# Performance work log

Hardware: AMD Instinct MI355X
Metric: run time of the kernel (lower is better)

## Reference

```python
import jax, jax.numpy as jnp
import numpy as np

N_NODES = 50000
N_EDGES = 800000
IN_FEATS = 256
OUT_FEATS = 64


def setup_inputs() -> dict:
    key = jax.random.key(0)
    k1, k2, k3, k4, k5 = jax.random.split(key, 5)
    h = jax.random.normal(k1, (N_NODES, IN_FEATS), dtype=jnp.float32)
    norm = jax.random.uniform(k2, (N_NODES,), dtype=jnp.float32)
    src = jax.random.randint(k3, (N_EDGES,), 0, N_NODES, dtype=jnp.int32)
    dst = jax.random.randint(k4, (N_EDGES,), 0, N_NODES, dtype=jnp.int32)
    # xavier_uniform for weight [in, out]
    limit = float(np.sqrt(6.0 / (IN_FEATS + OUT_FEATS)))
    weight = jax.random.uniform(k5, (IN_FEATS, OUT_FEATS), dtype=jnp.float32,
                                minval=-limit, maxval=limit)
    bias = jnp.zeros((OUT_FEATS,), dtype=jnp.float32)
    return {"h": h, "norm": norm, "src": src, "dst": dst,
            "weight": weight, "bias": bias}


def reference(h, norm, src, dst, weight, bias):
    # h: [N, in], weight: [in, out] -> projected node features [N, out]
    hw = jnp.matmul(h, weight)
    # message per edge: h_src * norm_src  -> [E, out]
    msg = hw[src] * norm[src][:, None]
    # sum over in-neighbors of each dst node -> [N, out]
    agg = jax.ops.segment_sum(msg, dst, num_segments=N_NODES)
    # scale by dst norm, add bias, activation
    out = agg * norm[:, None] + bias
    return jax.nn.relu(out)
```

## Files before the change

### kernel.cpp

```cpp
#include <hip/hip_runtime.h>

#define K_FEATS 256
#define C_FEATS 64
#define RCHUNK 1024
#define RROUNDS (RCHUNK / 64)
#define NDIGIT 512
#define DSHIFT 7
#define NMASK 127
#define LCAP 2560

typedef __attribute__((ext_vector_type(8))) short short8;
typedef __attribute__((ext_vector_type(8))) unsigned short ushort8;
typedef __attribute__((ext_vector_type(4))) float f32x4;

__device__ __forceinline__ unsigned short f2bf(float f) {
    union { float f; unsigned u; } v; v.f = f;
    unsigned r = v.u + 0x7FFF + ((v.u >> 16) & 1);
    return (unsigned short)(r >> 16);
}

__device__ __forceinline__ float bflo(unsigned u) { return __uint_as_float(u << 16); }
__device__ __forceinline__ float bfhi(unsigned u) { return __uint_as_float(u & 0xFFFF0000u); }


__global__ __launch_bounds__(256) void packhist_w_kernel(
    const int* __restrict__ dst, unsigned short* __restrict__ cm16,
    const float* __restrict__ w, unsigned short* __restrict__ wt,
    int n_edges, int nchunk)
{
    const int tid = threadIdx.x;
    if ((int)blockIdx.x < nchunk) {
        __shared__ unsigned cnt[NDIGIT];
        #pragma unroll
        for (int j = 0; j < NDIGIT / 256; ++j) cnt[tid + j * 256] = 0;
        __syncthreads();
        const int e0 = blockIdx.x * RCHUNK + tid * 4;
        if (e0 + 3 < n_edges) {
            const int4 d4 = *reinterpret_cast<const int4*>(dst + e0);
            atomicAdd(&cnt[d4.x >> DSHIFT], 1);
            atomicAdd(&cnt[d4.y >> DSHIFT], 1);
            atomicAdd(&cnt[d4.z >> DSHIFT], 1);
            atomicAdd(&cnt[d4.w >> DSHIFT], 1);
        } else {
            #pragma unroll
            for (int j = 0; j < 4; ++j) {
                if (e0 + j < n_edges) atomicAdd(&cnt[dst[e0 + j] >> DSHIFT], 1);
            }
        }
        __syncthreads();
        const unsigned o = cnt[tid * 2] | (cnt[tid * 2 + 1] << 16);
        reinterpret_cast<unsigned*>(cm16)[(size_t)blockIdx.x * (NDIGIT / 2) + tid] = o;
    } else {
        const int e2 = ((int)blockIdx.x - nchunk) * 1024 + tid;
        #pragma unroll
        for (int j = 0; j < 4; ++j) {
            const int idx = e2 + j * 256;
            const int col = idx >> 8, k = idx & 255;
            wt[idx] = f2bf(w[k * C_FEATS + col]);
        }
    }
}

__global__ __launch_bounds__(256) void scan_block_t_kernel(
    const unsigned short* __restrict__ cm16, int* __restrict__ out_dm,
    int* __restrict__ bsum, int n, int nchunk)
{
    __shared__ int s[256];
    const int tid = threadIdx.x;
    const int i = blockIdx.x * 256 + tid;
    int v = 0;
    if (i < n) {
        const int dig = i / nchunk;
        const int c   = i - dig * nchunk;
        v = (int)cm16[(size_t)c * NDIGIT + dig];
    }
    s[tid] = v;
    __syncthreads();
    #pragma unroll
    for (int d = 1; d < 256; d <<= 1) {
        int t = (tid >= d) ? s[tid - d] : 0;
        __syncthreads();
        s[tid] += t;
        __syncthreads();
    }
    if (i < n) out_dm[i] = s[tid] - v;
    if (tid == 255) bsum[blockIdx.x] = s[255];
}

__global__ __launch_bounds__(256) void scan_partials_digbase_kernel(
    int* __restrict__ bsum, int nb, const int* __restrict__ dm,
    int* __restrict__ digbase, int n_edges, int nchunk)
{
    __shared__ int s[256];
    const int tid = threadIdx.x;
    int v[16];
    int sum = 0;
    #pragma unroll
    for (int j = 0; j < 16; ++j) {
        const int i = tid * 16 + j;
        v[j] = (i < nb) ? bsum[i] : 0;
        sum += v[j];
    }
    s[tid] = sum;
    __syncthreads();
    #pragma unroll
    for (int d = 1; d < 256; d <<= 1) {
        int t = (tid >= d) ? s[tid - d] : 0;
        __syncthreads();
        s[tid] += t;
        __syncthreads();
    }
    int base = s[tid] - sum;
    #pragma unroll
    for (int j = 0; j < 16; ++j) {
        const int i = tid * 16 + j;
        if (i < nb) { bsum[i] = base; base += v[j]; }
    }
    __syncthreads();
    for (int g = tid; g < NDIGIT; g += 256) {
        const int gi = g * nchunk;
        digbase[g] = dm[gi] + bsum[gi >> 8];
    }
    if (tid == 0) digbase[NDIGIT] = n_edges;
}

__global__ __launch_bounds__(256) void reorder_gemm_kernel(
    const int* __restrict__ src, const int* __restrict__ dst,
    unsigned* __restrict__ P1, const int* __restrict__ dm,
    const int* __restrict__ bsum2,
    const float* __restrict__ h, const unsigned short* __restrict__ wt_g,
    const float* __restrict__ norm, unsigned short* __restrict__ hwn,
    int n_edges, int nchunk, int n_nodes, int nreb)
{
    __shared__ __align__(16) unsigned char lds[65536];
    const int tid = threadIdx.x;

    if ((int)blockIdx.x < nreb) {
        const int wv = tid >> 6;
        const int c = blockIdx.x * 4 + wv;
        if (c >= nchunk) return;
        unsigned* cnt = reinterpret_cast<unsigned*>(lds) + wv * NDIGIT;
        const int lane = tid & 63;
        #pragma unroll
        for (int j = 0; j < NDIGIT / 64; ++j) cnt[lane + j * 64] = 0;
        const int base = c * RCHUNK;

        unsigned dA = 0, sA = 0, dB = 0, sB = 0;
        if (base + lane < n_edges)      { dA = dst[base + lane];      sA = src[base + lane]; }
        if (base + 64 + lane < n_edges) { dB = dst[base + 64 + lane]; sB = src[base + 64 + lane]; }

        for (int r = 0; r < RROUNDS; ++r) {
            unsigned dC = 0, sC = 0;
            const int idxC = base + (r + 2) * 64 + lane;
            if (r + 2 < RROUNDS && idxC < n_edges) { dC = dst[idxC]; sC = src[idxC]; }

            const int idx = base + r * 64 + lane;
            const bool valid = idx < n_edges;
            const int g = valid ? (int)(dA >> DSHIFT) : NDIGIT;
            unsigned long long m = ~0ull;
            #pragma unroll
            for (int b = 0; b < 10; ++b) {
                const unsigned long long bb = __ballot((g >> b) & 1);
                m &= ((g >> b) & 1) ? bb : ~bb;
            }
            const unsigned long long below = m & ((1ull << lane) - 1ull);
            const int laneRank = __popcll(below);
            const int total = __popcll(m);
            const bool isFirst = (below == 0ull);
            if (valid) {
                const unsigned oldc = cnt[g];
                const int gi = g * nchunk + c;
                const unsigned slot = (unsigned)dm[gi] + (unsigned)bsum2[gi >> 8]
                                    + oldc + (unsigned)laneRank;
                P1[slot] = ((dA & (unsigned)NMASK) << 16) | sA;
                if (isFirst) cnt[g] = oldc + (unsigned)total;
            }
            dA = dB; sA = sB; dB = dC; sB = sC;
        }
    } else {
        const int row0 = ((int)blockIdx.x - nreb) * 64;

        #pragma unroll
        for (int j = 0; j < 8; ++j) {
            const int ch = j * 256 + tid;
            const int r = ch >> 5, k0 = (ch & 31) * 8;
            const int row = row0 + r;
            ushort8 v;
            if (row < n_nodes) {
                const float4 f0 = *reinterpret_cast<const float4*>(h + (size_t)row * K_FEATS + k0);
                const float4 f1 = *reinterpret_cast<const float4*>(h + (size_t)row * K_FEATS + k0 + 4);
                v[0]=f2bf(f0.x); v[1]=f2bf(f0.y); v[2]=f2bf(f0.z); v[3]=f2bf(f0.w);
                v[4]=f2bf(f1.x); v[5]=f2bf(f1.y); v[6]=f2bf(f1.z); v[7]=f2bf(f1.w);
            } else {
                v = (ushort8)0;
            }
            const int addr = (r * 512 + k0 * 2) ^ ((r & 7) << 4);
            *reinterpret_cast<ushort8*>(lds + addr) = v;
        }
        #pragma unroll
        for (int j = 0; j < 8; ++j) {
            const int ch = j * 256 + tid;
            const int col = ch >> 5, k0 = (ch & 31) * 8;
            const ushort8 v = *reinterpret_cast<const ushort8*>(wt_g + ch * 8);
            const int addr = 32768 + ((col * 512 + k0 * 2) ^ ((col & 7) << 4));
            *reinterpret_cast<ushort8*>(lds + addr) = v;
        }
        __syncthreads();

        const int lane = tid & 63, w = tid >> 6;
        const int r16 = lane & 15, kg = lane >> 4;
        const int x = (r16 & 7) << 4;

        f32x4 acc[4];
        #pragma unroll
        for (int n = 0; n < 4; ++n) acc[n] = (f32x4)0.f;

        #pragma unroll
        for (int kb = 0; kb < 8; ++kb) {
            const int common = (r16 * 512 + kb * 64 + kg * 16) ^ x;
            const short8 a = *reinterpret_cast<const short8*>(lds + w * 8192 + common);
            #pragma unroll
            for (int n = 0; n < 4; ++n) {
                const short8 b = *reinterpret_cast<const short8*>(lds + 32768 + n * 8192 + common);
                acc[n] = __builtin_amdgcn_mfma_f32_16x16x32_bf16(a, b, acc[n], 0, 0, 0);
            }
        }

        #pragma unroll
        for (int i = 0; i < 4; ++i) {
            const int row = row0 + w * 16 + kg * 4 + i;
            if (row < n_nodes) {
                const float nv = norm[row];
                #pragma unroll
                for (int n = 0; n < 4; ++n) {
                    hwn[(size_t)row * C_FEATS + n * 16 + r16] = f2bf(acc[n][i] * nv);
                }
            }
        }
    }
}

__global__ __launch_bounds__(512) void aggregate_kernel(
    const uint4* __restrict__ hwn4, const unsigned* __restrict__ P1,
    const int* __restrict__ digbase,
    const float* __restrict__ norm, const float* __restrict__ bias,
    float* __restrict__ out, int n_nodes)
{
    __shared__ unsigned stage[LCAP];
    __shared__ unsigned short lsrc[LCAP];
    __shared__ int cnt128[128];
    __shared__ int cur128[128];
    __shared__ int segbase[129];

    const int tid = threadIdx.x;
    const int b = blockIdx.x;
    const int n0 = b * 128;

    const int s = digbase[b];
    const int bucketsz = digbase[b + 1] - s;

    if (tid < 128) { cnt128[tid] = 0; cur128[tid] = 0; }
    __syncthreads();

    const int lane = tid & 63;
    const int wv = tid >> 6;
    const int q  = lane >> 3;
    const int c8 = lane & 7;

    if (bucketsz <= LCAP) {
        for (int i = tid; i < bucketsz; i += 512) {
            const unsigned key = P1[s + i];
            stage[i] = key;
            atomicAdd(&cnt128[key >> 16], 1);
        }
        __syncthreads();
        if (tid < 64) {
            const int a = cnt128[2 * tid], bb = cnt128[2 * tid + 1];
            int p = a + bb;
            #pragma unroll
            for (int d = 1; d < 64; d <<= 1) {
                const int t = __shfl_up(p, d);
                if (tid >= d) p += t;
            }
            segbase[2 * tid]     = p - a - bb;
            segbase[2 * tid + 1] = p - bb;
            if (tid == 63) segbase[128] = p;
        }
        __syncthreads();
        for (int i = tid; i < bucketsz; i += 512) {
            const unsigned key = stage[i];
            const int nn = key >> 16;
            const int pos = atomicAdd(&cur128[nn], 1);
            lsrc[segbase[nn] + pos] = (unsigned short)key;
        }
        __syncthreads();
        for (int nn = wv; nn < 128; nn += 8) {
            const int node = n0 + nn;
            if (node >= n_nodes) break;
            const int ls = segbase[nn];
            const int le = segbase[nn + 1];
            float a0=0.f,a1=0.f,a2=0.f,a3=0.f,a4=0.f,a5=0.f,a6=0.f,a7=0.f;
            int e = ls + q;
            for (; e + 8 < le; e += 16) {
                const uint4 u = hwn4[(size_t)lsrc[e] * 8 + c8];
                const uint4 v = hwn4[(size_t)lsrc[e + 8] * 8 + c8];
                a0 += bflo(u.x) + bflo(v.x); a1 += bfhi(u.x) + bfhi(v.x);
                a2 += bflo(u.y) + bflo(v.y); a3 += bfhi(u.y) + bfhi(v.y);
                a4 += bflo(u.z) + bflo(v.z); a5 += bfhi(u.z) + bfhi(v.z);
                a6 += bflo(u.w) + bflo(v.w); a7 += bfhi(u.w) + bfhi(v.w);
            }
            for (; e < le; e += 8) {
                const uint4 u = hwn4[(size_t)lsrc[e] * 8 + c8];
                a0 += bflo(u.x); a1 += bfhi(u.x);
                a2 += bflo(u.y); a3 += bfhi(u.y);
                a4 += bflo(u.z); a5 += bfhi(u.z);
                a6 += bflo(u.w); a7 += bfhi(u.w);
            }
            #pragma unroll
            for (int d = 8; d < 64; d <<= 1) {
                a0 += __shfl_xor(a0, d); a1 += __shfl_xor(a1, d);
                a2 += __shfl_xor(a2, d); a3 += __shfl_xor(a3, d);
                a4 += __shfl_xor(a4, d); a5 += __shfl_xor(a5, d);
                a6 += __shfl_xor(a6, d); a7 += __shfl_xor(a7, d);
            }
            if (q == 0) {
                const float nv = norm[node];
                const float4 b0 = *reinterpret_cast<const float4*>(bias + c8 * 8);
                const float4 b1 = *reinterpret_cast<const float4*>(bias + c8 * 8 + 4);
                float4 o0, o1;
                o0.x = fmaxf(fmaf(a0, nv, b0.x), 0.f);
                o0.y = fmaxf(fmaf(a1, nv, b0.y), 0.f);
                o0.z = fmaxf(fmaf(a2, nv, b0.z), 0.f);
                o0.w = fmaxf(fmaf(a3, nv, b0.w), 0.f);
                o1.x = fmaxf(fmaf(a4, nv, b1.x), 0.f);
                o1.y = fmaxf(fmaf(a5, nv, b1.y), 0.f);
                o1.z = fmaxf(fmaf(a6, nv, b1.z), 0.f);
                o1.w = fmaxf(fmaf(a7, nv, b1.w), 0.f);
                float* po = out + (size_t)node * C_FEATS + c8 * 8;
                *reinterpret_cast<float4*>(po)     = o0;
                *reinterpret_cast<float4*>(po + 4) = o1;
            }
        }
    } else {
        for (int nn = wv; nn < 128; nn += 8) {
            const int node = n0 + nn;
            if (node >= n_nodes) break;
            float a0=0.f,a1=0.f,a2=0.f,a3=0.f,a4=0.f,a5=0.f,a6=0.f,a7=0.f;
            for (int i = q; i < bucketsz; i += 8) {
                const unsigned key = P1[s + i];
                if ((int)(key >> 16) == nn) {
                    const uint4 u = hwn4[(size_t)(key & 0xFFFFu) * 8 + c8];
                    a0 += bflo(u.x); a1 += bfhi(u.x);
                    a2 += bflo(u.y); a3 += bfhi(u.y);
                    a4 += bflo(u.z); a5 += bfhi(u.z);
                    a6 += bflo(u.w); a7 += bfhi(u.w);
                }
            }
            #pragma unroll
            for (int d = 8; d < 64; d <<= 1) {
                a0 += __shfl_xor(a0, d); a1 += __shfl_xor(a1, d);
                a2 += __shfl_xor(a2, d); a3 += __shfl_xor(a3, d);
                a4 += __shfl_xor(a4, d); a5 += __shfl_xor(a5, d);
                a6 += __shfl_xor(a6, d); a7 += __shfl_xor(a7, d);
            }
            if (q == 0) {
                const float nv = norm[node];
                const float4 b0 = *reinterpret_cast<const float4*>(bias + c8 * 8);
                const float4 b1 = *reinterpret_cast<const float4*>(bias + c8 * 8 + 4);
                float4 o0, o1;
                o0.x = fmaxf(fmaf(a0, nv, b0.x), 0.f);
                o0.y = fmaxf(fmaf(a1, nv, b0.y), 0.f);
                o0.z = fmaxf(fmaf(a2, nv, b0.z), 0.f);
                o0.w = fmaxf(fmaf(a3, nv, b0.w), 0.f);
                o1.x = fmaxf(fmaf(a4, nv, b1.x), 0.f);
                o1.y = fmaxf(fmaf(a5, nv, b1.y), 0.f);
                o1.z = fmaxf(fmaf(a6, nv, b1.z), 0.f);
                o1.w = fmaxf(fmaf(a7, nv, b1.w), 0.f);
                float* po = out + (size_t)node * C_FEATS + c8 * 8;
                *reinterpret_cast<float4*>(po)     = o0;
                *reinterpret_cast<float4*>(po + 4) = o1;
            }
        }
    }
}

extern "C" void kernel_launch(void* const* d_in, const int* in_sizes, int n_in,
                              void* d_out, int out_size, void* d_ws, size_t ws_size,
                              hipStream_t stream) {
    const float* h      = (const float*)d_in[0];
    const float* norm   = (const float*)d_in[1];
    const int*   src    = (const int*)d_in[2];
    const int*   dst    = (const int*)d_in[3];
    const float* weight = (const float*)d_in[4];
    const float* bias   = (const float*)d_in[5];

    const int n_nodes = in_sizes[1];
    const int n_edges = in_sizes[2];

    char* ws = (char*)d_ws;
    unsigned* P1            = (unsigned*)(ws + 0);
    int* dm                 = (int*)(ws + 3200000);
    unsigned short* cm16    = (unsigned short*)(ws + 4801536);
    unsigned short* hwn     = (unsigned short*)(ws + 5602304);
    int* bsum2              = (int*)(ws + 12002304);
    int* digbase            = (int*)(ws + 12008560);
    unsigned short* wt_g    = (unsigned short*)(ws + 12010624);

    const int nchunk  = (n_edges + RCHUNK - 1) / RCHUNK;
    const int nscan   = NDIGIT * nchunk;
    const int nb_r    = (nscan + 255) / 256;
    const int ngroup  = (n_nodes + 127) / 128;
    const int nreb    = (nchunk + 3) / 4;
    const int ngemm   = (n_nodes + 63) / 64;

    packhist_w_kernel<<<nchunk + 16, 256, 0, stream>>>(dst, cm16, weight, wt_g,
                                                       n_edges, nchunk);
    scan_block_t_kernel<<<nb_r, 256, 0, stream>>>(cm16, dm, bsum2, nscan, nchunk);
    scan_partials_digbase_kernel<<<1, 256, 0, stream>>>(bsum2, nb_r, dm, digbase,
                                                        n_edges, nchunk);
    reorder_gemm_kernel<<<nreb + ngemm, 256, 0, stream>>>(
        src, dst, P1, dm, bsum2, h, wt_g, norm, hwn,
        n_edges, nchunk, n_nodes, nreb);
    aggregate_kernel<<<ngroup, 512, 0, stream>>>(
        (const uint4*)hwn, P1, digbase, norm, bias, (float*)d_out, n_nodes);
}
```

Measured before the change: 73.51 us.

## Replace two-pass global scan with per-bucket scan and in-kernel digit-base prefix

```diff
diff --git a/kernel.cpp b/kernel.cpp
--- a/kernel.cpp
+++ b/kernel.cpp
@@ -61,73 +61,44 @@
     }
 }
 
-__global__ __launch_bounds__(256) void scan_block_t_kernel(
-    const unsigned short* __restrict__ cm16, int* __restrict__ out_dm,
-    int* __restrict__ bsum, int n, int nchunk)
+__global__ __launch_bounds__(256) void bucketscan_kernel(
+    const unsigned short* __restrict__ cm16, int* __restrict__ dm,
+    int* __restrict__ totals, int nchunk)
 {
     __shared__ int s[256];
-    const int tid = threadIdx.x;
-    const int i = blockIdx.x * 256 + tid;
-    int v = 0;
-    if (i < n) {
-        const int dig = i / nchunk;
-        const int c   = i - dig * nchunk;
-        v = (int)cm16[(size_t)c * NDIGIT + dig];
-    }
-    s[tid] = v;
+    const int g = blockIdx.x;
+    const int t = threadIdx.x;
+    int v[4];
+    int sum = 0;
+    #pragma unroll
+    for (int j = 0; j < 4; ++j) {
+        const int c = t * 4 + j;
+        v[j] = (c < nchunk) ? (int)cm16[(size_t)c * NDIGIT + g] : 0;
+        sum += v[j];
+    }
+    s[t] = sum;
     __syncthreads();
     #pragma unroll
     for (int d = 1; d < 256; d <<= 1) {
-        int t = (tid >= d) ? s[tid - d] : 0;
-        __syncthreads();
-        s[tid] += t;
-        __syncthreads();
-    }
-    if (i < n) out_dm[i] = s[tid] - v;
-    if (tid == 255) bsum[blockIdx.x] = s[255];
-}
-
-__global__ __launch_bounds__(256) void scan_partials_digbase_kernel(
-    int* __restrict__ bsum, int nb, const int* __restrict__ dm,
-    int* __restrict__ digbase, int n_edges, int nchunk)
-{
-    __shared__ int s[256];
-    const int tid = threadIdx.x;
-    int v[16];
-    int sum = 0;
+        int x = (t >= d) ? s[t - d] : 0;
+        __syncthreads();
+        s[t] += x;
+        __syncthreads();
+    }
+    int base = s[t] - sum;
     #pragma unroll
-    for (int j = 0; j < 16; ++j) {
-        const int i = tid * 16 + j;
-        v[j] = (i < nb) ? bsum[i] : 0;
-        sum += v[j];
-    }
-    s[tid] = sum;
-    __syncthreads();
-    #pragma unroll
-    for (int d = 1; d < 256; d <<= 1) {
-        int t = (tid >= d) ? s[tid - d] : 0;
-        __syncthreads();
-        s[tid] += t;
-        __syncthreads();
-    }
-    int base = s[tid] - sum;
-    #pragma unroll
-    for (int j = 0; j < 16; ++j) {
-        const int i = tid * 16 + j;
-        if (i < nb) { bsum[i] = base; base += v[j]; }
-    }
-    __syncthreads();
-    for (int g = tid; g < NDIGIT; g += 256) {
-        const int gi = g * nchunk;
-        digbase[g] = dm[gi] + bsum[gi >> 8];
-    }
-    if (tid == 0) digbase[NDIGIT] = n_edges;
+    for (int j = 0; j < 4; ++j) {
+        const int c = t * 4 + j;
+        if (c < nchunk) dm[(size_t)g * nchunk + c] = base;
+        base += v[j];
+    }
+    if (t == 255) totals[g] = s[255];
 }
 
 __global__ __launch_bounds__(256) void reorder_gemm_kernel(
     const int* __restrict__ src, const int* __restrict__ dst,
     unsigned* __restrict__ P1, const int* __restrict__ dm,
-    const int* __restrict__ bsum2,
+    const int* __restrict__ totals,
     const float* __restrict__ h, const unsigned short* __restrict__ wt_g,
     const float* __restrict__ norm, unsigned short* __restrict__ hwn,
     int n_edges, int nchunk, int n_nodes, int nreb)
@@ -136,10 +107,30 @@
     const int tid = threadIdx.x;
 
     if ((int)blockIdx.x < nreb) {
+        unsigned* cntall  = reinterpret_cast<unsigned*>(lds);
+        int* ss           = reinterpret_cast<int*>(lds + 8192);
+        int* digbaseL     = reinterpret_cast<int*>(lds + 9216);
+        {
+            const int a  = totals[2 * tid];
+            const int b2 = totals[2 * tid + 1];
+            ss[tid] = a + b2;
+            __syncthreads();
+            #pragma unroll
+            for (int d = 1; d < 256; d <<= 1) {
+                int x = (tid >= d) ? ss[tid - d] : 0;
+                __syncthreads();
+                ss[tid] += x;
+                __syncthreads();
+            }
+            const int base = ss[tid] - (a + b2);
+            digbaseL[2 * tid]     = base;
+            digbaseL[2 * tid + 1] = base + a;
+            __syncthreads();
+        }
         const int wv = tid >> 6;
         const int c = blockIdx.x * 4 + wv;
         if (c >= nchunk) return;
-        unsigned* cnt = reinterpret_cast<unsigned*>(lds) + wv * NDIGIT;
+        unsigned* cnt = cntall + wv * NDIGIT;
         const int lane = tid & 63;
         #pragma unroll
         for (int j = 0; j < NDIGIT / 64; ++j) cnt[lane + j * 64] = 0;
@@ -169,8 +160,8 @@
             const bool isFirst = (below == 0ull);
             if (valid) {
                 const unsigned oldc = cnt[g];
-                const int gi = g * nchunk + c;
-                const unsigned slot = (unsigned)dm[gi] + (unsigned)bsum2[gi >> 8]
+                const unsigned slot = (unsigned)digbaseL[g]
+                                    + (unsigned)dm[(size_t)g * nchunk + c]
                                     + oldc + (unsigned)laneRank;
                 P1[slot] = ((dA & (unsigned)NMASK) << 16) | sA;
                 if (isFirst) cnt[g] = oldc + (unsigned)total;
@@ -242,25 +233,39 @@
 
 __global__ __launch_bounds__(512) void aggregate_kernel(
     const uint4* __restrict__ hwn4, const unsigned* __restrict__ P1,
-    const int* __restrict__ digbase,
+    const int* __restrict__ totals,
     const float* __restrict__ norm, const float* __restrict__ bias,
-    float* __restrict__ out, int n_nodes)
+    float* __restrict__ out, int n_nodes, int n_edges)
 {
     __shared__ unsigned stage[LCAP];
     __shared__ unsigned short lsrc[LCAP];
     __shared__ int cnt128[128];
     __shared__ int cur128[128];
     __shared__ int segbase[129];
+    __shared__ int ds[NDIGIT];
 
     const int tid = threadIdx.x;
     const int b = blockIdx.x;
     const int n0 = b * 128;
 
-    const int s = digbase[b];
-    const int bucketsz = digbase[b + 1] - s;
-
+    const int v = totals[tid];
+    ds[tid] = v;
+    __syncthreads();
+    #pragma unroll
+    for (int d = 1; d < NDIGIT; d <<= 1) {
+        int x = (tid >= d) ? ds[tid - d] : 0;
+        __syncthreads();
+        ds[tid] += x;
+        __syncthreads();
+    }
+    const int incl = ds[tid];
+    __syncthreads();
+    ds[tid] = incl - v;
     if (tid < 128) { cnt128[tid] = 0; cur128[tid] = 0; }
     __syncthreads();
+
+    const int s = ds[b];
+    const int bucketsz = ((b + 1 < NDIGIT) ? ds[b + 1] : n_edges) - s;
 
     const int lane = tid & 63;
     const int wv = tid >> 6;
@@ -303,11 +308,11 @@
             int e = ls + q;
             for (; e + 8 < le; e += 16) {
                 const uint4 u = hwn4[(size_t)lsrc[e] * 8 + c8];
-                const uint4 v = hwn4[(size_t)lsrc[e + 8] * 8 + c8];
-                a0 += bflo(u.x) + bflo(v.x); a1 += bfhi(u.x) + bfhi(v.x);
-                a2 += bflo(u.y) + bflo(v.y); a3 += bfhi(u.y) + bfhi(v.y);
-                a4 += bflo(u.z) + bflo(v.z); a5 += bfhi(u.z) + bfhi(v.z);
-                a6 += bflo(u.w) + bflo(v.w); a7 += bfhi(u.w) + bfhi(v.w);
+                const uint4 w2 = hwn4[(size_t)lsrc[e + 8] * 8 + c8];
+                a0 += bflo(u.x) + bflo(w2.x); a1 += bfhi(u.x) + bfhi(w2.x);
+                a2 += bflo(u.y) + bflo(w2.y); a3 += bfhi(u.y) + bfhi(w2.y);
+                a4 += bflo(u.z) + bflo(w2.z); a5 += bfhi(u.z) + bfhi(w2.z);
+                a6 += bflo(u.w) + bflo(w2.w); a7 += bfhi(u.w) + bfhi(w2.w);
             }
             for (; e < le; e += 8) {
                 const uint4 u = hwn4[(size_t)lsrc[e] * 8 + c8];
@@ -402,25 +407,20 @@
     int* dm                 = (int*)(ws + 3200000);
     unsigned short* cm16    = (unsigned short*)(ws + 4801536);
     unsigned short* hwn     = (unsigned short*)(ws + 5602304);
-    int* bsum2              = (int*)(ws + 12002304);
-    int* digbase            = (int*)(ws + 12008560);
-    unsigned short* wt_g    = (unsigned short*)(ws + 12010624);
+    int* totals             = (int*)(ws + 12002304);
+    unsigned short* wt_g    = (unsigned short*)(ws + 12004352);
 
     const int nchunk  = (n_edges + RCHUNK - 1) / RCHUNK;
-    const int nscan   = NDIGIT * nchunk;
-    const int nb_r    = (nscan + 255) / 256;
     const int ngroup  = (n_nodes + 127) / 128;
     const int nreb    = (nchunk + 3) / 4;
     const int ngemm   = (n_nodes + 63) / 64;
 
     packhist_w_kernel<<<nchunk + 16, 256, 0, stream>>>(dst, cm16, weight, wt_g,
                                                        n_edges, nchunk);
-    scan_block_t_kernel<<<nb_r, 256, 0, stream>>>(cm16, dm, bsum2, nscan, nchunk);
-    scan_partials_digbase_kernel<<<1, 256, 0, stream>>>(bsum2, nb_r, dm, digbase,
-                                                        n_edges, nchunk);
+    bucketscan_kernel<<<NDIGIT, 256, 0, stream>>>(cm16, dm, totals, nchunk);
     reorder_gemm_kernel<<<nreb + ngemm, 256, 0, stream>>>(
-        src, dst, P1, dm, bsum2, h, wt_g, norm, hwn,
+        src, dst, P1, dm, totals, h, wt_g, norm, hwn,
         n_edges, nchunk, n_nodes, nreb);
     aggregate_kernel<<<ngroup, 512, 0, stream>>>(
-        (const uint4*)hwn, P1, digbase, norm, bias, (float*)d_out, n_nodes);
-}
+        (const uint4*)hwn, P1, totals, norm, bias, (float*)d_out, n_nodes, n_edges);
+}
```

Measured after the change: 70.53 us (median of 2 runs). 1.04x faster.
